# Performance work log

Measured on AMD Instinct MI355X. Metric: run time of the kernel, lower is better.

Reference implementation:

```python
import jax, jax.numpy as jnp
import numpy as np

N_QUBITS = 7
N_LAYERS = 4
DIM = 2 ** N_QUBITS  # 128
# PennyLane StronglyEntanglingLayers default ranges: (l % (n_wires-1)) + 1
RANGES = [(l % (N_QUBITS - 1)) + 1 for l in range(N_LAYERS)]  # [1,2,3,4]
BATCH = 262144


def rot_matrix(phi, theta, omega):
    """PennyLane Rot(phi, theta, omega) = RZ(omega) RY(theta) RZ(phi)."""
    c = jnp.cos(theta / 2)
    s = jnp.sin(theta / 2)
    a = jnp.exp(-0.5j * (phi + omega)) * c
    b = -jnp.exp(0.5j * (phi - omega)) * s
    cc = jnp.exp(-0.5j * (phi - omega)) * s
    d = jnp.exp(0.5j * (phi + omega)) * c
    return jnp.stack([jnp.stack([a, b]), jnp.stack([cc, d])])  # (2,2) complex64


def apply_1q(psi, U, wire):
    # psi: (batch, 2,2,2,2,2,2,2); apply 2x2 U on qubit axis 1+wire
    psi = jnp.moveaxis(psi, 1 + wire, -1)
    psi = psi @ U.T
    return jnp.moveaxis(psi, -1, 1 + wire)


def apply_cnot(psi, ctrl, tgt):
    psi = jnp.moveaxis(psi, (1 + ctrl, 1 + tgt), (-2, -1))
    # flip target amplitude pair where control == 1
    psi = jnp.concatenate([psi[..., 0:1, :], psi[..., 1:2, ::-1]], axis=-2)
    return jnp.moveaxis(psi, (-2, -1), (1 + ctrl, 1 + tgt))


def setup_inputs() -> dict:
    key = jax.random.key(0)
    k1, k2 = jax.random.split(key)
    x = jax.random.normal(k1, (BATCH, DIM), dtype=jnp.float32)
    weights = jax.random.normal(k2, (N_LAYERS, N_QUBITS, 3), dtype=jnp.float32)
    return {"x": x, "weights": weights}


def reference(x, weights):
    # AmplitudeEmbedding with normalize=True
    norm = jnp.linalg.norm(x, axis=-1, keepdims=True)
    psi = (x / norm).astype(jnp.complex64)
    psi = psi.reshape((-1,) + (2,) * N_QUBITS)

    # StronglyEntanglingLayers
    for l in range(N_LAYERS):
        for w in range(N_QUBITS):
            U = rot_matrix(weights[l, w, 0], weights[l, w, 1], weights[l, w, 2])
            psi = apply_1q(psi, U, w)
        r = RANGES[l]
        for w in range(N_QUBITS):
            psi = apply_cnot(psi, w, (w + r) % N_QUBITS)

    # expval(Z0 @ Z6): sign = (-1)^(b0 + b6)
    probs = (jnp.abs(psi) ** 2).reshape(-1, 2, DIM // 4, 2)  # (batch, q0, mid, q6)
    z = jnp.array([1.0, -1.0], dtype=jnp.float32)
    return jnp.einsum('a,namb,b->n', z, probs, z)
```

## Files before the change

### kernel.cpp

```cpp
#include <hip/hip_runtime.h>


#define N_QUBITS 7
#define DIM 128
#define N_LAYERS 4
#define BATCH 262144
#define GRID 1024
#define ROWS 32
#define ITERS (BATCH / (GRID * ROWS))
#define DEPTH 2

typedef short short8 __attribute__((ext_vector_type(8)));
typedef float f32x4 __attribute__((ext_vector_type(4)));
typedef unsigned int u32;
typedef __attribute__((address_space(1))) const u32 g_u32;
typedef __attribute__((address_space(3))) u32 l_u32;

__device__ __forceinline__ unsigned short f2bf(float f) {
  unsigned u = __builtin_bit_cast(unsigned, f);
  u += 0x7fffu + ((u >> 16) & 1u);
  return (unsigned short)(u >> 16);
}

__device__ __forceinline__ unsigned pk2(float x, float y) {
  unsigned ux = __builtin_bit_cast(unsigned, x) + 0x8000u;
  unsigned uy = __builtin_bit_cast(unsigned, y) + 0x8000u;
  return __builtin_amdgcn_perm(uy, ux, 0x07060302u);
}

__device__ __forceinline__ short8 pack_bf16(float4 lo, float4 hi) {
  uint4 d;
  d.x = pk2(lo.x, lo.y);
  d.y = pk2(lo.z, lo.w);
  d.z = pk2(hi.x, hi.y);
  d.w = pk2(hi.z, hi.w);
  return __builtin_bit_cast(short8, d);
}

__global__ void sim_columns(const float* __restrict__ W,
                            float* __restrict__ Ur, float* __restrict__ Ui) {
  __shared__ float sr[DIM], si[DIM];
  const int c = blockIdx.x;
  const int t = threadIdx.x;

  sr[t] = (t == c) ? 1.f : 0.f;        si[t] = 0.f;
  sr[t + 64] = (t + 64 == c) ? 1.f : 0.f;  si[t + 64] = 0.f;
  __syncthreads();

  for (int l = 0; l < N_LAYERS; ++l) {
    for (int w = 0; w < N_QUBITS; ++w) {
      const float phi = W[(l * 7 + w) * 3 + 0];
      const float th  = W[(l * 7 + w) * 3 + 1];
      const float om  = W[(l * 7 + w) * 3 + 2];
      const float ch = __cosf(0.5f * th), sh = __sinf(0.5f * th);
      const float ap = 0.5f * (phi + om), am = 0.5f * (phi - om);
      const float cap = __cosf(ap), sap = __sinf(ap);
      const float cam = __cosf(am), sam = __sinf(am);
      const float ar =  cap * ch, ai = -sap * ch;
      const float br = -cam * sh, bi = -sam * sh;
      const float cr =  cam * sh, ci = -sam * sh;
      const float dr =  cap * ch, di =  sap * ch;

      const int m = 1 << (6 - w);
      const int i0 = ((t & ~(m - 1)) << 1) | (t & (m - 1));
      const int i1 = i0 | m;
      const float x0r = sr[i0], x0i = si[i0];
      const float x1r = sr[i1], x1i = si[i1];
      __syncthreads();
      sr[i0] = ar * x0r - ai * x0i + br * x1r - bi * x1i;
      si[i0] = ar * x0i + ai * x0r + br * x1i + bi * x1r;
      sr[i1] = cr * x0r - ci * x0i + dr * x1r - di * x1i;
      si[i1] = cr * x0i + ci * x0r + dr * x1i + di * x1r;
      __syncthreads();
    }
    const int r = (l % (N_QUBITS - 1)) + 1;
    for (int w = 0; w < N_QUBITS; ++w) {
      const int ctrl = w, tgt = (w + r) % N_QUBITS;
      const int cmask = 1 << (6 - ctrl), tmask = 1 << (6 - tgt);
      const int i0 = ((t & ~(tmask - 1)) << 1) | (t & (tmask - 1));
      const int i1 = i0 | tmask;
      const float a0r = sr[i0], a0i = si[i0];
      const float a1r = sr[i1], a1i = si[i1];
      __syncthreads();
      if (i0 & cmask) {
        sr[i0] = a1r; si[i0] = a1i;
        sr[i1] = a0r; si[i1] = a0i;
      }
      __syncthreads();
    }
  }
  Ur[(size_t)t * DIM + c]        = sr[t];
  Ui[(size_t)t * DIM + c]        = si[t];
  Ur[(size_t)(t + 64) * DIM + c] = sr[t + 64];
  Ui[(size_t)(t + 64) * DIM + c] = si[t + 64];
}

__global__ void build_A(const float* __restrict__ Ur, const float* __restrict__ Ui,
                        unsigned short* __restrict__ Ab) {
  const int i = blockIdx.x;
  const int j = threadIdx.x;
  float s = 0.f;
#pragma unroll 8
  for (int k = 0; k < DIM; ++k) {
    const float zk = (((k >> 6) ^ k) & 1) ? -1.f : 1.f;
    s += zk * (Ur[k * DIM + i] * Ur[k * DIM + j] + Ui[k * DIM + i] * Ui[k * DIM + j]);
  }
  Ab[i * DIM + j] = f2bf(s);
}

__device__ __forceinline__ void stage_half(const float* __restrict__ X, float* XsBuf,
                                           int tile, int wave, int lane) {
#pragma unroll
  for (int j = 0; j < 8; ++j) {
    const int s = 512 * wave + 64 * j + lane;
    const int row = s >> 5;
    const int c = (s & 31) ^ (row & 7);
    const float* gp = X + (size_t)tile * (ROWS * DIM) + row * DIM + c * 4;
    __builtin_amdgcn_global_load_lds((g_u32*)gp, (l_u32*)(XsBuf + s * 4), 16, 0, 0);
  }
}

__global__ __launch_bounds__(128, 2) void vqa_main(const float* __restrict__ X,
                                                   const unsigned short* __restrict__ Ab,
                                                   float* __restrict__ out) {
  __shared__ float Xs[DEPTH * ROWS * DIM];

  const int tid = threadIdx.x;
  const int lane = tid & 63;
  const int wave = tid >> 6;
  const int n16 = lane & 15;
  const int g = lane >> 4;
  const int R = 16 * wave + n16;
  const int rx = R & 7;

  short8 a_frag[4][8];
#pragma unroll
  for (int kt = 0; kt < 4; ++kt)
#pragma unroll
    for (int t = 0; t < 8; ++t)
      a_frag[kt][t] = *reinterpret_cast<const short8*>(
          Ab + (16 * t + n16) * DIM + 32 * kt + 8 * g);

  stage_half(X, Xs, blockIdx.x, wave, lane);

#pragma unroll 1
  for (int it = 0; it < ITERS; ++it) {
    const int cur = it & 1;

    if (it + 1 < ITERS) {
      stage_half(X, Xs + (cur ^ 1) * (ROWS * DIM),
                 blockIdx.x + (it + 1) * GRID, wave, lane);
      asm volatile("s_waitcnt vmcnt(8)" ::: "memory");
    } else {
      asm volatile("s_waitcnt vmcnt(0)" ::: "memory");
    }

    const int rb = cur * (ROWS * 32) + R * 32;

    short8 bfrag[4];
#pragma unroll
    for (int kt = 0; kt < 4; ++kt) {
      const int c0 = 8 * kt + 2 * g;
      const float4 lo = *reinterpret_cast<const float4*>(Xs + (rb + (c0 ^ rx)) * 4);
      const float4 hi = *reinterpret_cast<const float4*>(Xs + (rb + ((c0 + 1) ^ rx)) * 4);
      bfrag[kt] = pack_bf16(lo, hi);
    }

    f32x4 acc[8];
#pragma unroll
    for (int t = 0; t < 8; ++t) acc[t] = (f32x4){0.f, 0.f, 0.f, 0.f};
#pragma unroll
    for (int kt = 0; kt < 4; ++kt) {
#pragma unroll
      for (int t = 0; t < 8; ++t)
        acc[t] = __builtin_amdgcn_mfma_f32_16x16x32_bf16(a_frag[kt][t], bfrag[kt],
                                                         acc[t], 0, 0, 0);
    }

    float dot = 0.f, nrm = 0.f;
#pragma unroll
    for (int t = 0; t < 8; ++t) {
      const float4 xe = *reinterpret_cast<const float4*>(Xs + (rb + ((4 * t + g) ^ rx)) * 4);
      dot += xe.x * acc[t][0] + xe.y * acc[t][1] + xe.z * acc[t][2] + xe.w * acc[t][3];
      nrm += xe.x * xe.x + xe.y * xe.y + xe.z * xe.z + xe.w * xe.w;
    }
    dot += __shfl_xor(dot, 16, 64);
    dot += __shfl_xor(dot, 32, 64);
    nrm += __shfl_xor(nrm, 16, 64);
    nrm += __shfl_xor(nrm, 32, 64);
    if (g == 0) out[(blockIdx.x + it * GRID) * ROWS + R] = dot / nrm;
  }
}

extern "C" void kernel_launch(void* const* d_in, const int* in_sizes, int n_in,
                              void* d_out, int out_size, void* d_ws, size_t ws_size,
                              hipStream_t stream) {
  const float* X = (const float*)d_in[0];
  const float* W = (const float*)d_in[1];
  float* out = (float*)d_out;

  float* Ur = (float*)d_ws;
  float* Ui = Ur + DIM * DIM;
  unsigned short* Ab = (unsigned short*)(Ui + DIM * DIM);

  sim_columns<<<DIM, 64, 0, stream>>>(W, Ur, Ui);
  build_A<<<DIM, DIM, 0, stream>>>(Ur, Ui, Ab);
  vqa_main<<<GRID, 128, 0, stream>>>(X, Ab, out);
}
```

Baseline: 212.0 us.

## Keep A matrix in swizzled LDS instead of registers and halve grid

The 128x128 bf16 A operand is staged once per block into XOR-swizzled shared memory, and each iteration reads its MFMA fragments from there, instead of holding 128 VGPRs of fragments per lane. The grid drops from 1024 to 512 blocks, so each block handles more tiles and the per-block A staging cost is spread over more work. The X double-buffer prefetch is reorganised around a full vmcnt(0) wait plus a block barrier, and the next tile is issued after the B fragments are read. The aim is to cut register pressure and the repeated global loads of A, at the cost of extra LDS traffic per MFMA, a barrier every iteration, and 64KB of LDS per block.

```diff
diff --git a/kernel.cpp b/kernel.cpp
--- a/kernel.cpp
+++ b/kernel.cpp
@@ -5,10 +5,9 @@
 #define DIM 128
 #define N_LAYERS 4
 #define BATCH 262144
-#define GRID 1024
+#define GRID 512
 #define ROWS 32
 #define ITERS (BATCH / (GRID * ROWS))
-#define DEPTH 2
 
 typedef short short8 __attribute__((ext_vector_type(8)));
 typedef float f32x4 __attribute__((ext_vector_type(4)));
@@ -108,11 +107,11 @@
   Ab[i * DIM + j] = f2bf(s);
 }
 
-__device__ __forceinline__ void stage_half(const float* __restrict__ X, float* XsBuf,
-                                           int tile, int wave, int lane) {
+__device__ __forceinline__ void stage_tile(const float* __restrict__ X, float* XsBuf,
+                                           int tile, int tid) {
 #pragma unroll
   for (int j = 0; j < 8; ++j) {
-    const int s = 512 * wave + 64 * j + lane;
+    const int s = tid + 128 * j;
     const int row = s >> 5;
     const int c = (s & 31) ^ (row & 7);
     const float* gp = X + (size_t)tile * (ROWS * DIM) + row * DIM + c * 4;
@@ -123,39 +122,40 @@
 __global__ __launch_bounds__(128, 2) void vqa_main(const float* __restrict__ X,
                                                    const unsigned short* __restrict__ Ab,
                                                    float* __restrict__ out) {
-  __shared__ float Xs[DEPTH * ROWS * DIM];
+  __shared__ unsigned short As[DIM * DIM];
+  __shared__ float Xs[2 * ROWS * DIM];
 
   const int tid = threadIdx.x;
   const int lane = tid & 63;
   const int wave = tid >> 6;
   const int n16 = lane & 15;
   const int g = lane >> 4;
+
+  stage_tile(X, Xs, blockIdx.x, tid);
+
+#pragma unroll
+  for (int i = 0; i < 16; ++i) {
+    const int q = tid + 128 * i;
+    const int m = q >> 4, c = q & 15;
+    const short8 v = *reinterpret_cast<const short8*>(Ab + q * 8);
+    *reinterpret_cast<short8*>(As + m * DIM + ((c ^ (m & 15)) << 3)) = v;
+  }
+
+  const unsigned short* abase[4];
+#pragma unroll
+  for (int kt = 0; kt < 4; ++kt)
+    abase[kt] = As + n16 * DIM + (((4 * kt + g) ^ n16) << 3);
+
   const int R = 16 * wave + n16;
   const int rx = R & 7;
-
-  short8 a_frag[4][8];
-#pragma unroll
-  for (int kt = 0; kt < 4; ++kt)
-#pragma unroll
-    for (int t = 0; t < 8; ++t)
-      a_frag[kt][t] = *reinterpret_cast<const short8*>(
-          Ab + (16 * t + n16) * DIM + 32 * kt + 8 * g);
-
-  stage_half(X, Xs, blockIdx.x, wave, lane);
 
 #pragma unroll 1
   for (int it = 0; it < ITERS; ++it) {
     const int cur = it & 1;
-
-    if (it + 1 < ITERS) {
-      stage_half(X, Xs + (cur ^ 1) * (ROWS * DIM),
-                 blockIdx.x + (it + 1) * GRID, wave, lane);
-      asm volatile("s_waitcnt vmcnt(8)" ::: "memory");
-    } else {
-      asm volatile("s_waitcnt vmcnt(0)" ::: "memory");
-    }
-
     const int rb = cur * (ROWS * 32) + R * 32;
+
+    asm volatile("s_waitcnt vmcnt(0)" ::: "memory");
+    __syncthreads();
 
     short8 bfrag[4];
 #pragma unroll
@@ -166,15 +166,19 @@
       bfrag[kt] = pack_bf16(lo, hi);
     }
 
+    if (it + 1 < ITERS)
+      stage_tile(X, Xs + (cur ^ 1) * (ROWS * DIM), blockIdx.x + (it + 1) * GRID, tid);
+
     f32x4 acc[8];
 #pragma unroll
     for (int t = 0; t < 8; ++t) acc[t] = (f32x4){0.f, 0.f, 0.f, 0.f};
 #pragma unroll
     for (int kt = 0; kt < 4; ++kt) {
 #pragma unroll
-      for (int t = 0; t < 8; ++t)
-        acc[t] = __builtin_amdgcn_mfma_f32_16x16x32_bf16(a_frag[kt][t], bfrag[kt],
-                                                         acc[t], 0, 0, 0);
+      for (int t = 0; t < 8; ++t) {
+        const short8 af = *reinterpret_cast<const short8*>(abase[kt] + t * 16 * DIM);
+        acc[t] = __builtin_amdgcn_mfma_f32_16x16x32_bf16(af, bfrag[kt], acc[t], 0, 0, 0);
+      }
     }
 
     float dot = 0.f, nrm = 0.f;
@@ -188,7 +192,7 @@
     dot += __shfl_xor(dot, 32, 64);
     nrm += __shfl_xor(nrm, 16, 64);
     nrm += __shfl_xor(nrm, 32, 64);
-    if (g == 0) out[(blockIdx.x + it * GRID) * ROWS + R] = dot / nrm;
+    if (lane < 16) out[(blockIdx.x + it * GRID) * ROWS + R] = dot / nrm;
   }
 }
 
```

Result: faster. 204.3 us (-3.6%).
